# Optimization experiments

Measured on AMD Instinct MI355X. Metric: run time of the kernel, lower is better.

The kernel has to match this reference:

```python
import jax, jax.numpy as jnp
import numpy as np

D_MODEL = 1024
NHEAD = 16
D_HEAD = D_MODEL // NHEAD
B, L = 2, 2048


def setup_inputs() -> dict:
    key = jax.random.key(0)
    ks = jax.random.split(key, 11)
    s = 1.0 / np.sqrt(D_MODEL)
    return {
        "Q": jax.random.normal(ks[0], (B, L, D_MODEL), jnp.float32),
        "K": jax.random.normal(ks[1], (B, L, D_MODEL), jnp.float32),
        "V": jax.random.normal(ks[2], (B, L, D_MODEL), jnp.float32),
        "Wq": jax.random.normal(ks[3], (D_MODEL, D_MODEL), jnp.float32) * s,
        "bq": jax.random.normal(ks[4], (D_MODEL,), jnp.float32) * 0.01,
        "Wk": jax.random.normal(ks[5], (D_MODEL, D_MODEL), jnp.float32) * s,
        "bk": jax.random.normal(ks[6], (D_MODEL,), jnp.float32) * 0.01,
        "Wv": jax.random.normal(ks[7], (D_MODEL, D_MODEL), jnp.float32) * s,
        "bv": jax.random.normal(ks[8], (D_MODEL,), jnp.float32) * 0.01,
        "Wo": jax.random.normal(ks[9], (D_MODEL, D_MODEL), jnp.float32) * s,
        "bo": jax.random.normal(ks[10], (D_MODEL,), jnp.float32) * 0.01,
    }


def reference(Q, K, V, Wq, bq, Wk, bk, Wv, bv, Wo, bo):
    b, l, _ = Q.shape
    # QKV linear projections (nn.Linear: x @ W.T + b), then split into heads
    q = (Q @ Wq.T + bq).reshape(b, l, NHEAD, D_HEAD)
    k = (K @ Wk.T + bk).reshape(b, l, NHEAD, D_HEAD)
    v = (V @ Wv.T + bv).reshape(b, l, NHEAD, D_HEAD)
    # scaled dot-product attention: softmax(QK^T / sqrt(d_head)) V
    scale = jnp.asarray(1.0 / np.sqrt(D_HEAD), q.dtype)
    scores = jnp.einsum("bqhd,bkhd->bhqk", q, k) * scale  # [B,H,L,L]
    attn = jax.nn.softmax(scores, axis=-1)
    out = jnp.einsum("bhqk,bkhd->bqhd", attn, v)  # [B,L,H,Dh]
    out = out.reshape(b, l, D_MODEL)  # concat heads
    return out @ Wo.T + bo
```

## Files before the change

### kernel.cpp

```cpp
#include <hip/hip_runtime.h>
#include <cstdint>
#include <cstddef>

#define DM 1024
#define NH 16
#define DH 64
#define NB 2
#define SQ 2048
#define MT (NB*SQ)

typedef float  f32x4  __attribute__((ext_vector_type(4)));
typedef float  f32x16 __attribute__((ext_vector_type(16)));
typedef short  s16x8 __attribute__((ext_vector_type(8)));
typedef short  s16x4 __attribute__((ext_vector_type(4)));

__device__ __forceinline__ unsigned short f2bf(float x) {
    unsigned int u = __float_as_uint(x);
    unsigned int lsb = (u >> 16) & 1u;
    u += 0x7fffu + lsb;
    return (unsigned short)(u >> 16);
}

__device__ __forceinline__ unsigned int cvtpk(float lo, float hi) {
    unsigned int r;
    asm("v_cvt_pk_bf16_f32 %0, %1, %2" : "=v"(r) : "v"(lo), "v"(hi));
    return r;
}

__device__ __forceinline__ void gload16(const void* g, void* l) {
    __builtin_amdgcn_global_load_lds(
        (const __attribute__((address_space(1))) void*)g,
        (__attribute__((address_space(3))) void*)l,
        16, 0, 0);
}

#define BIGB (MT*DM/1024)
#define WB_B (DM*DM/1024)
__global__ __launch_bounds__(256) void castall(
    const float* __restrict__ s0, const float* __restrict__ s1, const float* __restrict__ s2,
    const float* __restrict__ s3, const float* __restrict__ s4, const float* __restrict__ s5,
    const float* __restrict__ s6,
    unsigned short* __restrict__ d0, unsigned short* __restrict__ d1,
    unsigned short* __restrict__ d2, unsigned short* __restrict__ d3,
    unsigned short* __restrict__ d4, unsigned short* __restrict__ d5,
    unsigned short* __restrict__ d6) {
    int bid = blockIdx.x;
    const float* src;
    unsigned short* dst;
    int off;
    if (bid < 3 * BIGB) {
        int seg = bid / BIGB;
        off = (bid - seg * BIGB) * 1024;
        src = (seg == 0) ? s0 : (seg == 1) ? s1 : s2;
        dst = (seg == 0) ? d0 : (seg == 1) ? d1 : d2;
    } else {
        int r = bid - 3 * BIGB;
        int seg = r / WB_B;
        off = (r - seg * WB_B) * 1024;
        src = (seg == 0) ? s3 : (seg == 1) ? s4 : (seg == 2) ? s5 : s6;
        dst = (seg == 0) ? d3 : (seg == 1) ? d4 : (seg == 2) ? d5 : d6;
    }
    int i = off + threadIdx.x * 4;
    float4 a = *reinterpret_cast<const float4*>(src + i);
    s16x4 rr;
    rr[0] = (short)f2bf(a.x);
    rr[1] = (short)f2bf(a.y);
    rr[2] = (short)f2bf(a.z);
    rr[3] = (short)f2bf(a.w);
    *reinterpret_cast<s16x4*>(dst + i) = rr;
}

__device__ __forceinline__ void gemm_core(const unsigned short* __restrict__ A,
                                          const unsigned short* __restrict__ Bm,
                                          int m0, int n0, int t,
                                          unsigned short (*As)[64],
                                          unsigned short (*Bs)[64],
                                          f32x4 acc[4][4]) {
    const int lane = t & 63, w = t >> 6;
    const int wm = (w >> 1) * 64, wn = (w & 1) * 64;
    const int lo = lane & 15, hi = lane >> 4;

    for (int k0 = 0; k0 < DM; k0 += 64) {
#pragma unroll
        for (int i = 0; i < 4; i++) {
            int c = i * 256 + t;
            int r = c >> 3, col = (c & 7) * 8;
            gload16(A  + (size_t)(m0 + r) * DM + k0 + col, &As[r][col]);
            gload16(Bm + (size_t)(n0 + r) * DM + k0 + col, &Bs[r][col]);
        }
        asm volatile("s_waitcnt vmcnt(0)" ::: "memory");
        __syncthreads();

#pragma unroll
        for (int kk = 0; kk < 64; kk += 32) {
            s16x8 a[4], b[4];
#pragma unroll
            for (int mi = 0; mi < 4; mi++)
                a[mi] = *reinterpret_cast<const s16x8*>(&As[wm + mi * 16 + lo][kk + hi * 8]);
#pragma unroll
            for (int ni = 0; ni < 4; ni++)
                b[ni] = *reinterpret_cast<const s16x8*>(&Bs[wn + ni * 16 + lo][kk + hi * 8]);
#pragma unroll
            for (int mi = 0; mi < 4; mi++)
#pragma unroll
                for (int ni = 0; ni < 4; ni++)
                    acc[mi][ni] = __builtin_amdgcn_mfma_f32_16x16x32_bf16(
                        a[mi], b[ni], acc[mi][ni], 0, 0, 0);
        }
        __syncthreads();
    }
}

__global__ __launch_bounds__(256, 3) void gemm_qkv(
    const unsigned short* __restrict__ Qb, const unsigned short* __restrict__ Kb,
    const unsigned short* __restrict__ Vb,
    const unsigned short* __restrict__ Wq, const unsigned short* __restrict__ Wk,
    const unsigned short* __restrict__ Wv,
    const float* __restrict__ bq, const float* __restrict__ bk, const float* __restrict__ bv,
    unsigned short* __restrict__ qp, unsigned short* __restrict__ kp,
    unsigned short* __restrict__ vt) {
    __shared__ __align__(16) unsigned short As[128][64];
    __shared__ __align__(16) unsigned short Bs[128][64];
    const int t = threadIdx.x;
    const int z = blockIdx.z;
    const unsigned short* A    = (z == 0) ? Qb : (z == 1) ? Kb : Vb;
    const unsigned short* Bm   = (z == 0) ? Wq : (z == 1) ? Wk : Wv;
    const float*          bias = (z == 0) ? bq : (z == 1) ? bk : bv;
    const int m0 = blockIdx.y * 128, n0 = blockIdx.x * 128;

    f32x4 acc[4][4] = {};
    gemm_core(A, Bm, m0, n0, t, As, Bs, acc);

    const int lane = t & 63, w = t >> 6;
    const int wm = (w >> 1) * 64, wn = (w & 1) * 64;
    const int lo = lane & 15, hi = lane >> 4;

    if (z < 2) {
        unsigned short* C = z ? kp : qp;
        const float scale = z ? 1.0f : 0.18033688011112042f;
#pragma unroll
        for (int mi = 0; mi < 4; mi++)
#pragma unroll
            for (int ni = 0; ni < 4; ni++) {
                int cc = n0 + wn + ni * 16 + lo;
                float bb = bias[cc];
#pragma unroll
                for (int j = 0; j < 4; j++) {
                    int rr = m0 + wm + mi * 16 + hi * 4 + j;
                    C[(size_t)rr * DM + cc] = f2bf((acc[mi][ni][j] + bb) * scale);
                }
            }
    } else {
#pragma unroll
        for (int mi = 0; mi < 4; mi++)
#pragma unroll
            for (int ni = 0; ni < 4; ni++) {
                int cc = n0 + wn + ni * 16 + lo;
                float bb = bias[cc];
                int rr0 = m0 + wm + mi * 16 + hi * 4;
                size_t base = ((size_t)(rr0 >> 11) * DM + cc) * SQ + (rr0 & (SQ - 1));
                s16x4 st;
#pragma unroll
                for (int j = 0; j < 4; j++)
                    st[j] = (short)f2bf(acc[mi][ni][j] + bb);
                *reinterpret_cast<s16x4*>(&vt[base]) = st;
            }
    }
}

__global__ __launch_bounds__(256, 3) void gemm_out(
    const unsigned short* __restrict__ Ao, const unsigned short* __restrict__ Wo,
    const float* __restrict__ bo, float* __restrict__ Cout) {
    __shared__ __align__(16) unsigned short As[128][64];
    __shared__ __align__(16) unsigned short Bs[128][64];
    const int t = threadIdx.x;
    const int m0 = blockIdx.y * 128, n0 = blockIdx.x * 128;

    f32x4 acc[4][4] = {};
    gemm_core(Ao, Wo, m0, n0, t, As, Bs, acc);

    const int lane = t & 63, w = t >> 6;
    const int wm = (w >> 1) * 64, wn = (w & 1) * 64;
    const int lo = lane & 15, hi = lane >> 4;
#pragma unroll
    for (int mi = 0; mi < 4; mi++)
#pragma unroll
        for (int ni = 0; ni < 4; ni++) {
            int cc = n0 + wn + ni * 16 + lo;
            float bb = bo[cc];
#pragma unroll
            for (int j = 0; j < 4; j++) {
                int rr = m0 + wm + mi * 16 + hi * 4 + j;
                Cout[(size_t)rr * DM + cc] = acc[mi][ni][j] + bb;
            }
        }
}

__global__ __launch_bounds__(256, 2) void attn_k(
    const unsigned short* __restrict__ qp, const unsigned short* __restrict__ kp,
    const unsigned short* __restrict__ vt, unsigned short* __restrict__ ao) {
    __shared__ __align__(16) unsigned short Ks[2][128][64];
    __shared__ __align__(16) unsigned short Vs[2][64][128];

    const int t = threadIdx.x;
    const int lane = t & 63, w = t >> 6;
    const int l5 = lane & 31, hb = lane >> 5;
    const int q0 = blockIdx.x * 128;
    const int bh = blockIdx.y;
    const int b = bh >> 4, h = bh & 15;

    const unsigned short* qrow = qp + (size_t)(b * SQ + q0 + w * 32 + l5) * DM + h * DH;
    s16x8 qfrag[4];
#pragma unroll
    for (int kk = 0; kk < 4; kk++)
        qfrag[kk] = *reinterpret_cast<const s16x8*>(qrow + kk * 16 + hb * 8);

    auto stage = [&](int bufi, int kt) {
#pragma unroll
        for (int i = 0; i < 4; i++) {
            int c = i * 256 + t;
            int r = c >> 3, col = ((c & 7) ^ (r & 7)) * 8;
            gload16(kp + (size_t)(b * SQ + kt + r) * DM + h * DH + col,
                    &Ks[bufi][r][(c & 7) * 8]);
        }
#pragma unroll
        for (int i = 0; i < 4; i++) {
            int c = i * 256 + t;
            int r = c >> 4, col = ((c & 15) ^ (r & 15)) * 8;
            gload16(vt + (size_t)(bh * DH + r) * SQ + kt + col,
                    &Vs[bufi][r][(c & 15) * 8]);
        }
    };

    float mrow = -1e30f, lrow = 0.0f;
    f32x16 oaccT[2] = {};

    stage(0, 0);
    int cur = 0;
    const int NT = SQ / 128;

    for (int ti = 0; ti < NT; ti++) {
        if (ti + 1 < NT) {
            stage(cur ^ 1, (ti + 1) * 128);
            asm volatile("s_waitcnt vmcnt(8)" ::: "memory");
        } else {
            asm volatile("s_waitcnt vmcnt(0)" ::: "memory");
        }
        __builtin_amdgcn_sched_barrier(0);
        __builtin_amdgcn_s_barrier();

        f32x16 sT[4] = {};
        __builtin_amdgcn_s_setprio(1);
#pragma unroll
        for (int ks = 0; ks < 4; ks++) {
#pragma unroll
            for (int kk = 0; kk < 4; kk++) {
                int kr = ks * 32 + l5;
                s16x8 kf = *reinterpret_cast<const s16x8*>(
                    &Ks[cur][kr][((kk * 2 + hb) ^ (kr & 7)) * 8]);
                sT[ks] = __builtin_amdgcn_mfma_f32_32x32x16_bf16(
                    kf, qfrag[kk], sT[ks], 0, 0, 0);
            }
        }
        __builtin_amdgcn_s_setprio(0);

        float mx = -3.0e38f;
#pragma unroll
        for (int ks = 0; ks < 4; ks++) {
            float t0 = fmaxf(fmaxf(sT[ks][0], sT[ks][1]), sT[ks][2]);
            float t1 = fmaxf(fmaxf(sT[ks][3], sT[ks][4]), sT[ks][5]);
            float t2 = fmaxf(fmaxf(sT[ks][6], sT[ks][7]), sT[ks][8]);
            float t3 = fmaxf(fmaxf(sT[ks][9], sT[ks][10]), sT[ks][11]);
            float t4 = fmaxf(fmaxf(sT[ks][12], sT[ks][13]), sT[ks][14]);
            float t5 = fmaxf(fmaxf(sT[ks][15], t0), t1);
            float t6 = fmaxf(fmaxf(t2, t3), t4);
            mx = fmaxf(fmaxf(mx, t5), t6);
        }
        mx = fmaxf(mx, __shfl_xor(mx, 32));

        if (!__all(mx <= mrow + 8.0f)) {
            float mnew = fmaxf(mrow, mx);
            float fs = exp2f(mrow - mnew);
            mrow = mnew;
            lrow *= fs;
            oaccT[0] *= fs;
            oaccT[1] *= fs;
        }

        float ps0 = 0.0f, ps1 = 0.0f, ps2 = 0.0f, ps3 = 0.0f;
#pragma unroll
        for (int ks = 0; ks < 4; ks++)
#pragma unroll
            for (int r = 0; r < 16; r += 4) {
                float e0 = exp2f(sT[ks][r]     - mrow);
                float e1 = exp2f(sT[ks][r + 1] - mrow);
                float e2 = exp2f(sT[ks][r + 2] - mrow);
                float e3 = exp2f(sT[ks][r + 3] - mrow);
                sT[ks][r] = e0; sT[ks][r + 1] = e1;
                sT[ks][r + 2] = e2; sT[ks][r + 3] = e3;
                ps0 += e0; ps1 += e1; ps2 += e2; ps3 += e3;
            }
        float ps = (ps0 + ps1) + (ps2 + ps3);
        ps += __shfl_xor(ps, 32);
        lrow += ps;

#pragma unroll
        for (int ks = 0; ks < 4; ks++) {
            unsigned int pw0[4], pw1[4];
#pragma unroll
            for (int m = 0; m < 4; m++) {
                pw0[m] = cvtpk(sT[ks][4 * m], sT[ks][4 * m + 1]);
                pw1[m] = cvtpk(sT[ks][4 * m + 2], sT[ks][4 * m + 3]);
            }
#pragma unroll
            for (int tt = 0; tt < 2; tt++) {
                unsigned int s0 = hb ? pw0[2 * tt] : pw0[2 * tt + 1];
                unsigned int s1 = hb ? pw1[2 * tt] : pw1[2 * tt + 1];
                unsigned int r0 = __shfl_xor(s0, 32);
                unsigned int r1 = __shfl_xor(s1, 32);
                union { unsigned int u[4]; s16x8 v; } uu;
                if (hb == 0) { uu.u[0] = pw0[2 * tt]; uu.u[1] = pw1[2 * tt];
                               uu.u[2] = r0;          uu.u[3] = r1; }
                else         { uu.u[0] = r0;          uu.u[1] = r1;
                               uu.u[2] = pw0[2 * tt + 1]; uu.u[3] = pw1[2 * tt + 1]; }
                s16x8 pf = uu.v;
                __builtin_amdgcn_s_setprio(1);
#pragma unroll
                for (int dblk = 0; dblk < 2; dblk++) {
                    int vr = dblk * 32 + l5;
                    int sl = ((ks * 2 + tt) * 2 + hb) ^ (vr & 15);
                    s16x8 vf = *reinterpret_cast<const s16x8*>(&Vs[cur][vr][sl * 8]);
                    oaccT[dblk] = __builtin_amdgcn_mfma_f32_32x32x16_bf16(
                        vf, pf, oaccT[dblk], 0, 0, 0);
                }
                __builtin_amdgcn_s_setprio(0);
            }
        }

        __builtin_amdgcn_s_barrier();
        cur ^= 1;
    }

    float inv = 1.0f / lrow;
    size_t rowbase = (size_t)(b * SQ + q0 + w * 32 + l5) * DM + h * DH;
#pragma unroll
    for (int dblk = 0; dblk < 2; dblk++)
#pragma unroll
        for (int g = 0; g < 4; g++) {
            unsigned int w0 = cvtpk(oaccT[dblk][4 * g] * inv, oaccT[dblk][4 * g + 1] * inv);
            unsigned int w1 = cvtpk(oaccT[dblk][4 * g + 2] * inv, oaccT[dblk][4 * g + 3] * inv);
            uint2 st = make_uint2(w0, w1);
            *reinterpret_cast<uint2*>(&ao[rowbase + dblk * 32 + 8 * g + 4 * hb]) = st;
        }
}

extern "C" void kernel_launch(void* const* d_in, const int* in_sizes, int n_in,
                              void* d_out, int out_size, void* d_ws, size_t ws_size,
                              hipStream_t stream) {
    const float* Q  = (const float*)d_in[0];
    const float* K  = (const float*)d_in[1];
    const float* V  = (const float*)d_in[2];
    const float* Wq = (const float*)d_in[3];
    const float* bq = (const float*)d_in[4];
    const float* Wk = (const float*)d_in[5];
    const float* bk = (const float*)d_in[6];
    const float* Wv = (const float*)d_in[7];
    const float* bv = (const float*)d_in[8];
    const float* Wo = (const float*)d_in[9];
    const float* bo = (const float*)d_in[10];

    char* ws = (char*)d_ws;
    size_t off = 0;
    auto alloc = [&](size_t bytes) {
        void* p = ws + off;
        off += (bytes + 255) & ~(size_t)255;
        return p;
    };
    const size_t XB = (size_t)MT * DM * 2;
    const size_t WB = (size_t)DM * DM * 2;
    unsigned short* qb  = (unsigned short*)alloc(XB);
    unsigned short* kb  = (unsigned short*)alloc(XB);
    unsigned short* vb  = (unsigned short*)alloc(XB);
    unsigned short* wqb = (unsigned short*)alloc(WB);
    unsigned short* wkb = (unsigned short*)alloc(WB);
    unsigned short* wvb = (unsigned short*)alloc(WB);
    unsigned short* wob = (unsigned short*)alloc(WB);
    unsigned short* qp  = (unsigned short*)alloc(XB);
    unsigned short* kp  = (unsigned short*)alloc(XB);
    unsigned short* vtp = (unsigned short*)alloc(XB);
    unsigned short* ao  = (unsigned short*)alloc(XB);

    castall<<<dim3(3 * BIGB + 4 * WB_B), 256, 0, stream>>>(
        Q, K, V, Wq, Wk, Wv, Wo, qb, kb, vb, wqb, wkb, wvb, wob);

    gemm_qkv<<<dim3(DM / 128, MT / 128, 3), 256, 0, stream>>>(
        qb, kb, vb, wqb, wkb, wvb, bq, bk, bv, qp, kp, vtp);

    attn_k<<<dim3(SQ / 128, NB * NH), 256, 0, stream>>>(qp, kp, vtp, ao);

    gemm_out<<<dim3(DM / 128, MT / 128), 256, 0, stream>>>(ao, wob, bo, (float*)d_out);
}
```

Before: 254.2 us.

## Split attention over the key dimension with a separate combine kernel

Splits the key/value sequence into two halves along a new grid z dimension, so twice as many attention blocks run. Each half writes a partial bf16 output plus its row max and sum, and a new combine kernel merges them with a log-sum-exp reweighting. Double-buffered LDS staging is dropped in favour of single buffers with a full wait each tile, and launch bounds raise occupancy to 4 blocks. The risks are the loss of load/compute overlap, an extra kernel launch, extra memory traffic for the partials, and extra bf16 rounding in the partial outputs. Scratch buffers are reused for the partials.

```diff
diff --git a/kernel.cpp b/kernel.cpp
--- a/kernel.cpp
+++ b/kernel.cpp
@@ -19,6 +19,10 @@
     unsigned int lsb = (u >> 16) & 1u;
     u += 0x7fffu + lsb;
     return (unsigned short)(u >> 16);
+}
+
+__device__ __forceinline__ float bf2f(unsigned short u) {
+    return __uint_as_float(((unsigned int)u) << 16);
 }
 
 __device__ __forceinline__ unsigned int cvtpk(float lo, float hi) {
@@ -196,11 +200,12 @@
         }
 }
 
-__global__ __launch_bounds__(256, 2) void attn_k(
+__global__ __launch_bounds__(256, 4) void attn_k(
     const unsigned short* __restrict__ qp, const unsigned short* __restrict__ kp,
-    const unsigned short* __restrict__ vt, unsigned short* __restrict__ ao) {
-    __shared__ __align__(16) unsigned short Ks[2][128][64];
-    __shared__ __align__(16) unsigned short Vs[2][64][128];
+    const unsigned short* __restrict__ vt,
+    unsigned short* __restrict__ op, float* __restrict__ mlp) {
+    __shared__ __align__(16) unsigned short Ks[128][64];
+    __shared__ __align__(16) unsigned short Vs[64][128];
 
     const int t = threadIdx.x;
     const int lane = t & 63, w = t >> 6;
@@ -208,6 +213,8 @@
     const int q0 = blockIdx.x * 128;
     const int bh = blockIdx.y;
     const int b = bh >> 4, h = bh & 15;
+    const int z = blockIdx.z;
+    const int kt0 = z * (SQ / 2);
 
     const unsigned short* qrow = qp + (size_t)(b * SQ + q0 + w * 32 + l5) * DM + h * DH;
     s16x8 qfrag[4];
@@ -215,39 +222,25 @@
     for (int kk = 0; kk < 4; kk++)
         qfrag[kk] = *reinterpret_cast<const s16x8*>(qrow + kk * 16 + hb * 8);
 
-    auto stage = [&](int bufi, int kt) {
+    float mrow = -1e30f, lrow = 0.0f;
+    f32x16 oaccT[2] = {};
+
+    for (int ti = 0; ti < SQ / 256; ti++) {
+        int kt = kt0 + ti * 128;
 #pragma unroll
         for (int i = 0; i < 4; i++) {
             int c = i * 256 + t;
             int r = c >> 3, col = ((c & 7) ^ (r & 7)) * 8;
-            gload16(kp + (size_t)(b * SQ + kt + r) * DM + h * DH + col,
-                    &Ks[bufi][r][(c & 7) * 8]);
+            gload16(kp + (size_t)(b * SQ + kt + r) * DM + h * DH + col, &Ks[r][(c & 7) * 8]);
         }
 #pragma unroll
         for (int i = 0; i < 4; i++) {
             int c = i * 256 + t;
             int r = c >> 4, col = ((c & 15) ^ (r & 15)) * 8;
-            gload16(vt + (size_t)(bh * DH + r) * SQ + kt + col,
-                    &Vs[bufi][r][(c & 15) * 8]);
-        }
-    };
-
-    float mrow = -1e30f, lrow = 0.0f;
-    f32x16 oaccT[2] = {};
-
-    stage(0, 0);
-    int cur = 0;
-    const int NT = SQ / 128;
-
-    for (int ti = 0; ti < NT; ti++) {
-        if (ti + 1 < NT) {
-            stage(cur ^ 1, (ti + 1) * 128);
-            asm volatile("s_waitcnt vmcnt(8)" ::: "memory");
-        } else {
-            asm volatile("s_waitcnt vmcnt(0)" ::: "memory");
-        }
-        __builtin_amdgcn_sched_barrier(0);
-        __builtin_amdgcn_s_barrier();
+            gload16(vt + (size_t)(bh * DH + r) * SQ + kt + col, &Vs[r][(c & 15) * 8]);
+        }
+        asm volatile("s_waitcnt vmcnt(0)" ::: "memory");
+        __syncthreads();
 
         f32x16 sT[4] = {};
         __builtin_amdgcn_s_setprio(1);
@@ -257,7 +250,7 @@
             for (int kk = 0; kk < 4; kk++) {
                 int kr = ks * 32 + l5;
                 s16x8 kf = *reinterpret_cast<const s16x8*>(
-                    &Ks[cur][kr][((kk * 2 + hb) ^ (kr & 7)) * 8]);
+                    &Ks[kr][((kk * 2 + hb) ^ (kr & 7)) * 8]);
                 sT[ks] = __builtin_amdgcn_mfma_f32_32x32x16_bf16(
                     kf, qfrag[kk], sT[ks], 0, 0, 0);
             }
@@ -329,20 +322,19 @@
                 for (int dblk = 0; dblk < 2; dblk++) {
                     int vr = dblk * 32 + l5;
                     int sl = ((ks * 2 + tt) * 2 + hb) ^ (vr & 15);
-                    s16x8 vf = *reinterpret_cast<const s16x8*>(&Vs[cur][vr][sl * 8]);
+                    s16x8 vf = *reinterpret_cast<const s16x8*>(&Vs[vr][sl * 8]);
                     oaccT[dblk] = __builtin_amdgcn_mfma_f32_32x32x16_bf16(
                         vf, pf, oaccT[dblk], 0, 0, 0);
                 }
                 __builtin_amdgcn_s_setprio(0);
             }
         }
-
-        __builtin_amdgcn_s_barrier();
-        cur ^= 1;
+        __syncthreads();
     }
 
+    int grow = b * SQ + q0 + w * 32 + l5;
     float inv = 1.0f / lrow;
-    size_t rowbase = (size_t)(b * SQ + q0 + w * 32 + l5) * DM + h * DH;
+    size_t rowbase = (size_t)z * MT * DM + (size_t)grow * DM + h * DH;
 #pragma unroll
     for (int dblk = 0; dblk < 2; dblk++)
 #pragma unroll
@@ -350,8 +342,37 @@
             unsigned int w0 = cvtpk(oaccT[dblk][4 * g] * inv, oaccT[dblk][4 * g + 1] * inv);
             unsigned int w1 = cvtpk(oaccT[dblk][4 * g + 2] * inv, oaccT[dblk][4 * g + 3] * inv);
             uint2 st = make_uint2(w0, w1);
-            *reinterpret_cast<uint2*>(&ao[rowbase + dblk * 32 + 8 * g + 4 * hb]) = st;
-        }
+            *reinterpret_cast<uint2*>(&op[rowbase + dblk * 32 + 8 * g + 4 * hb]) = st;
+        }
+    if (hb == 0) {
+        size_t mi = ((size_t)z * MT + grow) * NH + h;
+        mlp[mi * 2 + 0] = mrow;
+        mlp[mi * 2 + 1] = lrow;
+    }
+}
+
+__global__ __launch_bounds__(256) void combine_k(
+    const unsigned short* __restrict__ op, const float* __restrict__ mlp,
+    unsigned short* __restrict__ ao) {
+    int row = blockIdx.x;
+    int d0 = threadIdx.x * 4;
+    int h = d0 >> 6;
+    size_t mi1 = ((size_t)row) * NH + h;
+    size_t mi2 = ((size_t)MT + row) * NH + h;
+    float m1 = mlp[mi1 * 2], l1 = mlp[mi1 * 2 + 1];
+    float m2 = mlp[mi2 * 2], l2 = mlp[mi2 * 2 + 1];
+    float M = fmaxf(m1, m2);
+    float w1 = l1 * exp2f(m1 - M), w2 = l2 * exp2f(m2 - M);
+    float inv = 1.0f / (w1 + w2);
+    w1 *= inv; w2 *= inv;
+    size_t i1 = (size_t)row * DM + d0;
+    s16x4 a = *reinterpret_cast<const s16x4*>(&op[i1]);
+    s16x4 bb = *reinterpret_cast<const s16x4*>(&op[(size_t)MT * DM + i1]);
+    unsigned int o0 = cvtpk(bf2f((unsigned short)a[0]) * w1 + bf2f((unsigned short)bb[0]) * w2,
+                            bf2f((unsigned short)a[1]) * w1 + bf2f((unsigned short)bb[1]) * w2);
+    unsigned int o1 = cvtpk(bf2f((unsigned short)a[2]) * w1 + bf2f((unsigned short)bb[2]) * w2,
+                            bf2f((unsigned short)a[3]) * w1 + bf2f((unsigned short)bb[3]) * w2);
+    *reinterpret_cast<uint2*>(&ao[i1]) = make_uint2(o0, o1);
 }
 
 extern "C" void kernel_launch(void* const* d_in, const int* in_sizes, int n_in,
@@ -390,13 +411,18 @@
     unsigned short* vtp = (unsigned short*)alloc(XB);
     unsigned short* ao  = (unsigned short*)alloc(XB);
 
+    unsigned short* op  = qb;
+    float*          mlp = (float*)vb;
+
     castall<<<dim3(3 * BIGB + 4 * WB_B), 256, 0, stream>>>(
         Q, K, V, Wq, Wk, Wv, Wo, qb, kb, vb, wqb, wkb, wvb, wob);
 
     gemm_qkv<<<dim3(DM / 128, MT / 128, 3), 256, 0, stream>>>(
         qb, kb, vb, wqb, wkb, wvb, bq, bk, bv, qp, kp, vtp);
 
-    attn_k<<<dim3(SQ / 128, NB * NH), 256, 0, stream>>>(qp, kp, vtp, ao);
+    attn_k<<<dim3(SQ / 128, NB * NH, 2), 256, 0, stream>>>(qp, kp, vtp, op, mlp);
+
+    combine_k<<<dim3(MT), 256, 0, stream>>>(op, mlp, ao);
 
     gemm_out<<<dim3(DM / 128, MT / 128), 256, 0, stream>>>(ao, wob, bo, (float*)d_out);
 }
```

After: 308.7 us. 21.4% more time.
